# Kernel tuning notes

Measured on AMD Instinct MI355X. Metric: run time of the kernel, lower is better.

Reference implementation:

```python
import jax, jax.numpy as jnp
import numpy as np

NUM_HEAD = 16

def setup_inputs() -> dict:
    key = jax.random.key(0)
    ks = jax.random.split(key, 5)
    B, S, E = 2, 2048, 1024
    x = jax.random.normal(ks[0], (B, S, E), dtype=jnp.float32)
    w_qkv = jax.random.normal(ks[1], (3 * E, E), dtype=jnp.float32) * (E ** -0.5)
    b_qkv = jax.random.normal(ks[2], (3 * E,), dtype=jnp.float32) * 0.01
    w_out = jax.random.normal(ks[3], (E, E), dtype=jnp.float32) * (E ** -0.5)
    b_out = jax.random.normal(ks[4], (E,), dtype=jnp.float32) * 0.01
    return {"x": x, "w_qkv": w_qkv, "b_qkv": b_qkv, "w_out": w_out, "b_out": b_out}

def reference(x, w_qkv, b_qkv, w_out, b_out):
    B, S, E = x.shape
    H = NUM_HEAD
    D = E // H
    # fused QKV projection (torch Linear: x @ W^T + b)
    qkv = x @ w_qkv.T + b_qkv                       # [B, S, 3E]
    qkv = qkv.reshape(B, S, 3, H, D).transpose(2, 0, 3, 1, 4)  # [3, B, H, S, D]
    q, k, v = qkv[0], qkv[1], qkv[2]
    # NOTE: source scales by sqrt(embed_size), not sqrt(head_dim)
    scale = jnp.asarray(E, x.dtype) ** 0.5
    att = jnp.einsum('bhqd,bhkd->bhqk', q, k) / scale   # [B, H, S, S]
    # NOTE: source applies softmax over dim=1 (the head axis) — replicated faithfully
    att = jax.nn.softmax(att, axis=1)
    ctx = jnp.einsum('bhqk,bhkd->bhqd', att, v)         # [B, H, S, D]
    ctx = ctx.transpose(0, 2, 1, 3).reshape(B, S, E)    # [B, S, E]
    return ctx @ w_out.T + b_out
```

## Files before the change

kernel.cpp:

```cpp
#include <hip/hip_runtime.h>
#include <hip/hip_bf16.h>
#include <stdint.h>

typedef float  f32x4  __attribute__((ext_vector_type(4)));
typedef short  bf16x8 __attribute__((ext_vector_type(8)));
typedef short  bf16x4 __attribute__((ext_vector_type(4)));
typedef unsigned short u16x8 __attribute__((ext_vector_type(8)));

#define MFMA16(a, b, c) __builtin_amdgcn_mfma_f32_16x16x32_bf16((a), (b), (c), 0, 0, 0)

#if __has_builtin(__builtin_amdgcn_mfma_f32_16x16x16bf16_1k)
#define MFMA16K16(a, b, c) __builtin_amdgcn_mfma_f32_16x16x16bf16_1k((a), (b), (c), 0, 0, 0)
#else
__device__ __forceinline__ f32x4 mfma16k16_asm(bf16x4 a, bf16x4 b, f32x4 c) {
  f32x4 d;
  asm volatile("v_mfma_f32_16x16x16_bf16 %0, %1, %2, %3"
               : "=v"(d) : "v"(a), "v"(b), "v"(c));
  return d;
}
#define MFMA16K16(a, b, c) mfma16k16_asm((a), (b), (c))
#endif

__device__ __forceinline__ void gload16(const void* g, void* l) {
  __builtin_amdgcn_global_load_lds((const __attribute__((address_space(1))) void*)g,
                                   (__attribute__((address_space(3))) void*)l,
                                   16, 0, 0);
}

__device__ __forceinline__ unsigned short bf16bits(float f) {
  __hip_bfloat16 h = __float2bfloat16(f);
  return *(unsigned short*)&h;
}

__device__ __forceinline__ float bf2f(unsigned short u) {
  unsigned int x = ((unsigned int)u) << 16;
  return *(float*)&x;
}

__device__ __forceinline__ void block_sync_lds() {
  asm volatile("s_waitcnt lgkmcnt(0)" ::: "memory");
  __builtin_amdgcn_s_barrier();
  asm volatile("" ::: "memory");
}

__device__ __forceinline__ void fence_order() { asm volatile("" ::: "memory"); }

__global__ void cast_kernel(const float* __restrict__ s, __hip_bfloat16* __restrict__ d, int n4) {
  int i = blockIdx.x * blockDim.x + threadIdx.x;
  if (i < n4) {
    float4 v = ((const float4*)s)[i];
    ushort4 u;
    u.x = bf16bits(v.x); u.y = bf16bits(v.y); u.z = bf16bits(v.z); u.w = bf16bits(v.w);
    ((ushort4*)d)[i] = u;
  }
}

__global__ __launch_bounds__(256) void gemm_qkv_kernel(
    const __hip_bfloat16* __restrict__ A,
    const __hip_bfloat16* __restrict__ B,
    const float* __restrict__ bias,
    __hip_bfloat16* __restrict__ Qo,
    __hip_bfloat16* __restrict__ Ko,
    __hip_bfloat16* __restrict__ Vt) {
  const int K = 1024;
  __shared__ __align__(16) __hip_bfloat16 As[128 * 32];
  __shared__ __align__(16) __hip_bfloat16 Bs[128 * 32];
  const int t = threadIdx.x;
  const int lane = t & 63, wv = t >> 6;
  const int wm = (wv >> 1) * 64, wn = (wv & 1) * 64;
  const int lr = lane & 15, lq = lane >> 4;
  const int m0 = blockIdx.y * 128, n0 = blockIdx.x * 128;

  f32x4 acc[4][4] = {};

  const int arow = t >> 2;
  const int acol = (t & 3) * 8;
  const __hip_bfloat16* Ag = A + (long)(m0 + arow) * K + acol;
  const __hip_bfloat16* Bg = B + (long)(n0 + arow) * K + acol;
  __hip_bfloat16* Asl = As + t * 8;
  __hip_bfloat16* Bsl = Bs + t * 8;

  for (int kk = 0; kk < K; kk += 32) {
    gload16(Ag + kk, Asl);
    gload16(Ag + kk + 64 * K, Asl + 2048);
    gload16(Bg + kk, Bsl);
    gload16(Bg + kk + 64 * K, Bsl + 2048);
    __syncthreads();
    bf16x8 af[4], bf[4];
#pragma unroll
    for (int i = 0; i < 4; ++i)
      af[i] = *(const bf16x8*)&As[(wm + i * 16 + lr) * 32 + lq * 8];
#pragma unroll
    for (int j = 0; j < 4; ++j)
      bf[j] = *(const bf16x8*)&Bs[(wn + j * 16 + lr) * 32 + lq * 8];
#pragma unroll
    for (int i = 0; i < 4; ++i)
#pragma unroll
      for (int j = 0; j < 4; ++j)
        acc[i][j] = MFMA16(af[i], bf[j], acc[i][j]);
    __syncthreads();
  }

#pragma unroll
  for (int i = 0; i < 4; ++i) {
#pragma unroll
    for (int j = 0; j < 4; ++j) {
      int col = n0 + wn + j * 16 + lr;
      int tsel = col >> 10, rem = col & 1023;
      int h = rem >> 6, d = rem & 63;
      float bs = bias[col];
      int rowb = m0 + wm + i * 16 + lq * 4;
#pragma unroll
      for (int r = 0; r < 4; ++r) {
        int m = rowb + r;
        int b = m >> 11, sdx = m & 2047;
        __hip_bfloat16 v = __float2bfloat16(acc[i][j][r] + bs);
        long bh = (long)(b * 16 + h);
        if (tsel == 0)       Qo[(bh * 2048 + sdx) * 64 + d] = v;
        else if (tsel == 1)  Ko[(bh * 2048 + sdx) * 64 + d] = v;
        else                 Vt[((bh * 128 + (sdx >> 4)) * 64 + d) * 16 + (sdx & 15)] = v;
      }
    }
  }
}

__global__ __launch_bounds__(512, 2) void attn_kernel(
    const __hip_bfloat16* __restrict__ Q,
    const __hip_bfloat16* __restrict__ K,
    const __hip_bfloat16* __restrict__ Vt,
    __hip_bfloat16* __restrict__ part) {
  __shared__ __align__(16) __hip_bfloat16 KsA[16 * 16 * 64];
  __shared__ __align__(16) __hip_bfloat16 KsB[16 * 16 * 64];
  __shared__ __align__(16) float psum[2 * 8 * 16 * 16];

  const int t = threadIdx.x, lane = t & 63, wv = t >> 6;
  const int lr = lane & 15, lq = lane >> 4;
  const int h0 = wv * 2;
  const int combo = blockIdx.x & 7;
  const int b = combo & 1, chunk = combo >> 1;
  const int q0 = (blockIdx.x >> 3) * 32;
  const int k0 = chunk * 512;
  const float c = 0.03125f * 1.44269504f;
  const long bh16 = (long)(b * 16);
  const int rot = ((lq + lr) & 3) * 4;

  auto stageK = [&](__hip_bfloat16* dst, int kks) {
#pragma unroll
    for (int cc = 0; cc < 4; ++cc) {
      const int p = cc * 8192 + t * 16;
      const int rho = p >> 7;
      const int hh = rho >> 4, kl = rho & 15;
      const int g = ((p >> 4) & 7) ^ (rho & 7);
      const __hip_bfloat16* src = K + ((bh16 + hh) * 2048 + kks + kl) * 64 + g * 8;
      gload16(src, (char*)dst + p);
    }
    fence_order();
  };

  bf16x8 qf[2][2][2];
#pragma unroll
  for (int hh = 0; hh < 2; ++hh)
#pragma unroll
    for (int qt = 0; qt < 2; ++qt)
#pragma unroll
      for (int dh = 0; dh < 2; ++dh)
        qf[hh][qt][dh] = *(const bf16x8*)(
            Q + ((bh16 + h0 + hh) * 2048 + q0 + qt * 16 + lr) * 64 + dh * 32 + lq * 8);

  stageK(KsA, k0);
  asm volatile("s_waitcnt vmcnt(0)" ::: "memory");
  block_sync_lds();

  f32x4 ctx[2][2][4] = {};

  auto body = [&](const __hip_bfloat16* Kc, __hip_bfloat16* Kn, int kt) {
    const int kb = chunk * 32 + kt;
    bf16x4 vg[2][4];
#pragma unroll
    for (int hh = 0; hh < 2; ++hh) {
      const __hip_bfloat16* vb = Vt + ((bh16 + h0 + hh) * 128 + kb) * 1024;
#pragma unroll
      for (int dt = 0; dt < 4; ++dt)
        vg[hh][dt] = *(const bf16x4*)(vb + (dt * 16 + lr) * 16 + lq * 4);
    }
    if (kt < 31) stageK(Kn, k0 + kt * 16 + 16);
    f32x4 s[2][2];
    __builtin_amdgcn_s_setprio(1);
#pragma unroll
    for (int hh = 0; hh < 2; ++hh) {
      const int rho = (h0 + hh) * 16 + lr;
      const __hip_bfloat16* kr = Kc + rho * 64;
      bf16x8 kf0 = *(const bf16x8*)(kr + ((lq ^ (rho & 7)) << 3));
      bf16x8 kf1 = *(const bf16x8*)(kr + (((lq + 4) ^ (rho & 7)) << 3));
#pragma unroll
      for (int qt = 0; qt < 2; ++qt) {
        f32x4 a = {};
        a = MFMA16(kf0, qf[hh][qt][0], a);
        a = MFMA16(kf1, qf[hh][qt][1], a);
        s[hh][qt] = a;
      }
    }
    __builtin_amdgcn_s_setprio(0);
#pragma unroll
    for (int qt = 0; qt < 2; ++qt) {
      f32x4 pp;
#pragma unroll
      for (int r = 0; r < 4; ++r) {
        s[0][qt][r] = __builtin_amdgcn_exp2f(s[0][qt][r] * c);
        s[1][qt][r] = __builtin_amdgcn_exp2f(s[1][qt][r] * c);
        pp[r] = s[0][qt][r] + s[1][qt][r];
      }
      *(f32x4*)&psum[qt * 2048 + wv * 256 + lr * 16 + rot] = pp;
    }
    block_sync_lds();
    if (wv < 2) {
      f32x4 tot = {};
#pragma unroll
      for (int w2 = 0; w2 < 8; ++w2)
        tot += *(const f32x4*)&psum[wv * 2048 + w2 * 256 + lr * 16 + rot];
      f32x4 inv;
#pragma unroll
      for (int r = 0; r < 4; ++r) inv[r] = __builtin_amdgcn_rcpf(tot[r]);
      *(f32x4*)&psum[wv * 2048 + lr * 16 + rot] = inv;
    }
    asm volatile("s_waitcnt vmcnt(0)" ::: "memory");
    block_sync_lds();
    __builtin_amdgcn_s_setprio(1);
    f32x4 inv0 = *(const f32x4*)&psum[lr * 16 + rot];
    f32x4 inv1 = *(const f32x4*)&psum[2048 + lr * 16 + rot];
#pragma unroll
    for (int hh = 0; hh < 2; ++hh) {
#pragma unroll
      for (int qt = 0; qt < 2; ++qt) {
        const f32x4 iv = qt ? inv1 : inv0;
        bf16x4 p4;
#pragma unroll
        for (int r = 0; r < 4; ++r) p4[r] = (short)bf16bits(s[hh][qt][r] * iv[r]);
#pragma unroll
        for (int dt = 0; dt < 4; ++dt)
          ctx[hh][qt][dt] = MFMA16K16(vg[hh][dt], p4, ctx[hh][qt][dt]);
      }
    }
    __builtin_amdgcn_s_setprio(0);
  };

#pragma unroll 1
  for (int kp = 0; kp < 16; ++kp) {
    body(KsA, KsB, 2 * kp);
    body(KsB, KsA, 2 * kp + 1);
  }

  unsigned short* Pc = (unsigned short*)KsA;
#pragma unroll
  for (int qt = 0; qt < 2; ++qt) {
    if (qt) block_sync_lds();
#pragma unroll
    for (int hh = 0; hh < 2; ++hh) {
      const int h = h0 + hh;
#pragma unroll
      for (int dt = 0; dt < 4; ++dt) {
        bf16x4 pk;
#pragma unroll
        for (int r = 0; r < 4; ++r) pk[r] = (short)bf16bits(ctx[hh][qt][dt][r]);
        const int o = h * 128 + dt * 32 + lq * 8;
        *(bf16x4*)((char*)Pc + lr * 2048 + (o ^ ((lr & 7) << 4))) = pk;
      }
    }
    block_sync_lds();
    unsigned short* gbase = (unsigned short*)part +
        ((long)(chunk * 4096 + b * 2048 + q0 + qt * 16)) * 1024;
#pragma unroll
    for (int j = 0; j < 4; ++j) {
      int gf = (j * 512 + t) * 8;
      int q = gf >> 10, hd = gf & 1023;
      u16x8 v = *(const u16x8*)((char*)Pc + q * 2048 + ((hd * 2) ^ ((q & 7) << 4)));
      *(u16x8*)&gbase[gf] = v;
    }
  }
}

__global__ void reduce_cast_kernel(const unsigned short* __restrict__ part,
                                   __hip_bfloat16* __restrict__ dst) {
  int i = blockIdx.x * blockDim.x + threadIdx.x;
  const long S4 = (long)4096 * 1024 / 4;
  const ushort4* p = (const ushort4*)part;
  float sx = 0.f, sy = 0.f, sz = 0.f, sw = 0.f;
#pragma unroll
  for (int c = 0; c < 4; ++c) {
    ushort4 v = p[i + c * S4];
    sx += bf2f(v.x); sy += bf2f(v.y); sz += bf2f(v.z); sw += bf2f(v.w);
  }
  ushort4 u;
  u.x = bf16bits(sx); u.y = bf16bits(sy); u.z = bf16bits(sz); u.w = bf16bits(sw);
  ((ushort4*)dst)[i] = u;
}

__global__ __launch_bounds__(256) void gemm_out_kernel(
    const __hip_bfloat16* __restrict__ A,
    const __hip_bfloat16* __restrict__ B,
    const float* __restrict__ bias,
    float* __restrict__ out) {
  const int K = 1024;
  __shared__ __align__(16) __hip_bfloat16 As[128 * 32];
  __shared__ __align__(16) __hip_bfloat16 Bs[128 * 32];
  const int t = threadIdx.x;
  const int lane = t & 63, wv = t >> 6;
  const int wm = (wv >> 1) * 64, wn = (wv & 1) * 64;
  const int lr = lane & 15, lq = lane >> 4;
  const int m0 = blockIdx.y * 128, n0 = blockIdx.x * 128;

  f32x4 acc[4][4] = {};

  const int arow = t >> 2;
  const int acol = (t & 3) * 8;
  const __hip_bfloat16* Ag = A + (long)(m0 + arow) * K + acol;
  const __hip_bfloat16* Bg = B + (long)(n0 + arow) * K + acol;
  __hip_bfloat16* Asl = As + t * 8;
  __hip_bfloat16* Bsl = Bs + t * 8;

  for (int kk = 0; kk < K; kk += 32) {
    gload16(Ag + kk, Asl);
    gload16(Ag + kk + 64 * K, Asl + 2048);
    gload16(Bg + kk, Bsl);
    gload16(Bg + kk + 64 * K, Bsl + 2048);
    __syncthreads();
    bf16x8 af[4], bf[4];
#pragma unroll
    for (int i = 0; i < 4; ++i)
      af[i] = *(const bf16x8*)&As[(wm + i * 16 + lr) * 32 + lq * 8];
#pragma unroll
    for (int j = 0; j < 4; ++j)
      bf[j] = *(const bf16x8*)&Bs[(wn + j * 16 + lr) * 32 + lq * 8];
#pragma unroll
    for (int i = 0; i < 4; ++i)
#pragma unroll
      for (int j = 0; j < 4; ++j)
        acc[i][j] = MFMA16(af[i], bf[j], acc[i][j]);
    __syncthreads();
  }

#pragma unroll
  for (int i = 0; i < 4; ++i) {
#pragma unroll
    for (int j = 0; j < 4; ++j) {
      int col = n0 + wn + j * 16 + lr;
      float bs = bias[col];
      int rowb = m0 + wm + i * 16 + lq * 4;
#pragma unroll
      for (int r = 0; r < 4; ++r) {
        out[(long)(rowb + r) * 1024 + col] = acc[i][j][r] + bs;
      }
    }
  }
}

extern "C" void kernel_launch(void* const* d_in, const int* in_sizes, int n_in,
                              void* d_out, int out_size, void* d_ws, size_t ws_size,
                              hipStream_t stream) {
  const float* x     = (const float*)d_in[0];
  const float* w_qkv = (const float*)d_in[1];
  const float* b_qkv = (const float*)d_in[2];
  const float* w_out = (const float*)d_in[3];
  const float* b_out = (const float*)d_in[4];
  float* out = (float*)d_out;
  char* ws = (char*)d_ws;

  __hip_bfloat16* xb    = (__hip_bfloat16*)(ws);
  __hip_bfloat16* wqkvb = (__hip_bfloat16*)(ws + (8ul << 20));
  __hip_bfloat16* woutb = (__hip_bfloat16*)(ws + (14ul << 20));
  __hip_bfloat16* Qb    = (__hip_bfloat16*)(ws + (16ul << 20));
  __hip_bfloat16* Kb    = (__hip_bfloat16*)(ws + (24ul << 20));
  __hip_bfloat16* Vtb   = (__hip_bfloat16*)(ws + (32ul << 20));
  __hip_bfloat16* partb = (__hip_bfloat16*)(ws + (40ul << 20));
  __hip_bfloat16* ctxb  = (__hip_bfloat16*)(ws + (72ul << 20));

  cast_kernel<<<4096, 256, 0, stream>>>(x, xb, 4194304 / 4);
  cast_kernel<<<3072, 256, 0, stream>>>(w_qkv, wqkvb, 3145728 / 4);
  cast_kernel<<<1024, 256, 0, stream>>>(w_out, woutb, 1048576 / 4);
  gemm_qkv_kernel<<<dim3(24, 32), 256, 0, stream>>>(xb, wqkvb, b_qkv, Qb, Kb, Vtb);
  attn_kernel<<<512, 512, 0, stream>>>(Qb, Kb, Vtb, partb);
  reduce_cast_kernel<<<4096, 256, 0, stream>>>((const unsigned short*)partb, ctxb);
  gemm_out_kernel<<<dim3(8, 32), 256, 0, stream>>>(ctxb, woutb, b_out, out);
}
```

Before: 268.6 us.

## Load K fragments directly to registers with pre-tiled K layout, drop LDS staging

The QKV GEMM now writes K in a tiled layout that matches the MFMA fragment order, so the attention kernel loads K straight from global memory into registers instead of staging it through double-buffered LDS with global_load_lds. K and V fragments are register double-buffered and prefetched after the QK MFMAs. The softmax-over-heads reduction now has every wave compute the reciprocal sums itself, using double-buffered padded psum. That removes the second barrier and the vmcnt wait per step. This raises register pressure and issues more scattered global loads per wave in exchange for fewer barriers and less LDS traffic.

```diff
diff --git a/kernel.cpp b/kernel.cpp
--- a/kernel.cpp
+++ b/kernel.cpp
@@ -42,8 +42,6 @@
   __builtin_amdgcn_s_barrier();
   asm volatile("" ::: "memory");
 }
-
-__device__ __forceinline__ void fence_order() { asm volatile("" ::: "memory"); }
 
 __global__ void cast_kernel(const float* __restrict__ s, __hip_bfloat16* __restrict__ d, int n4) {
   int i = blockIdx.x * blockDim.x + threadIdx.x;
@@ -116,9 +114,14 @@
         int b = m >> 11, sdx = m & 2047;
         __hip_bfloat16 v = __float2bfloat16(acc[i][j][r] + bs);
         long bh = (long)(b * 16 + h);
-        if (tsel == 0)       Qo[(bh * 2048 + sdx) * 64 + d] = v;
-        else if (tsel == 1)  Ko[(bh * 2048 + sdx) * 64 + d] = v;
-        else                 Vt[((bh * 128 + (sdx >> 4)) * 64 + d) * 16 + (sdx & 15)] = v;
+        if (tsel == 0) {
+          Qo[(bh * 2048 + sdx) * 64 + d] = v;
+        } else if (tsel == 1) {
+          Ko[(bh * 128 + (sdx >> 4)) * 1024 + (d >> 5) * 512 +
+             ((d >> 3) & 3) * 128 + (sdx & 15) * 8 + (d & 7)] = v;
+        } else {
+          Vt[((bh * 128 + (sdx >> 4)) * 64 + d) * 16 + (sdx & 15)] = v;
+        }
       }
     }
   }
@@ -129,9 +132,8 @@
     const __hip_bfloat16* __restrict__ K,
     const __hip_bfloat16* __restrict__ Vt,
     __hip_bfloat16* __restrict__ part) {
-  __shared__ __align__(16) __hip_bfloat16 KsA[16 * 16 * 64];
-  __shared__ __align__(16) __hip_bfloat16 KsB[16 * 16 * 64];
-  __shared__ __align__(16) float psum[2 * 8 * 16 * 16];
+  __shared__ float psum[2][5120];
+  __shared__ __align__(16) unsigned short epi[16 * 1024];
 
   const int t = threadIdx.x, lane = t & 63, wv = t >> 6;
   const int lr = lane & 15, lq = lane >> 4;
@@ -139,23 +141,10 @@
   const int combo = blockIdx.x & 7;
   const int b = combo & 1, chunk = combo >> 1;
   const int q0 = (blockIdx.x >> 3) * 32;
-  const int k0 = chunk * 512;
+  const int kb0 = chunk * 32;
   const float c = 0.03125f * 1.44269504f;
   const long bh16 = (long)(b * 16);
-  const int rot = ((lq + lr) & 3) * 4;
-
-  auto stageK = [&](__hip_bfloat16* dst, int kks) {
-#pragma unroll
-    for (int cc = 0; cc < 4; ++cc) {
-      const int p = cc * 8192 + t * 16;
-      const int rho = p >> 7;
-      const int hh = rho >> 4, kl = rho & 15;
-      const int g = ((p >> 4) & 7) ^ (rho & 7);
-      const __hip_bfloat16* src = K + ((bh16 + hh) * 2048 + kks + kl) * 64 + g * 8;
-      gload16(src, (char*)dst + p);
-    }
-    fence_order();
-  };
+  const int poff = lr * 20 + lq * 4;
 
   bf16x8 qf[2][2][2];
 #pragma unroll
@@ -167,40 +156,43 @@
         qf[hh][qt][dh] = *(const bf16x8*)(
             Q + ((bh16 + h0 + hh) * 2048 + q0 + qt * 16 + lr) * 64 + dh * 32 + lq * 8);
 
-  stageK(KsA, k0);
-  asm volatile("s_waitcnt vmcnt(0)" ::: "memory");
-  block_sync_lds();
+  bf16x8 kfA[2][2], kfB[2][2];
+  bf16x4 vgA[2][4], vgB[2][4];
+
+  auto loadKV = [&](bf16x8 (&KF)[2][2], bf16x4 (&VG)[2][4], int kb) {
+#pragma unroll
+    for (int hh = 0; hh < 2; ++hh) {
+      const __hip_bfloat16* kptr =
+          K + ((bh16 + h0 + hh) * 128 + kb) * 1024 + lq * 128 + lr * 8;
+      KF[hh][0] = *(const bf16x8*)kptr;
+      KF[hh][1] = *(const bf16x8*)(kptr + 512);
+      const __hip_bfloat16* vptr =
+          Vt + ((bh16 + h0 + hh) * 128 + kb) * 1024 + lr * 16 + lq * 4;
+#pragma unroll
+      for (int dt = 0; dt < 4; ++dt)
+        VG[hh][dt] = *(const bf16x4*)(vptr + dt * 256);
+    }
+  };
+
+  loadKV(kfA, vgA, kb0);
 
   f32x4 ctx[2][2][4] = {};
 
-  auto body = [&](const __hip_bfloat16* Kc, __hip_bfloat16* Kn, int kt) {
-    const int kb = chunk * 32 + kt;
-    bf16x4 vg[2][4];
-#pragma unroll
-    for (int hh = 0; hh < 2; ++hh) {
-      const __hip_bfloat16* vb = Vt + ((bh16 + h0 + hh) * 128 + kb) * 1024;
-#pragma unroll
-      for (int dt = 0; dt < 4; ++dt)
-        vg[hh][dt] = *(const bf16x4*)(vb + (dt * 16 + lr) * 16 + lq * 4);
-    }
-    if (kt < 31) stageK(Kn, k0 + kt * 16 + 16);
+  auto body = [&](bf16x8 (&KF)[2][2], bf16x4 (&VG)[2][4],
+                  bf16x8 (&KFN)[2][2], bf16x4 (&VGN)[2][4], int kt, int par) {
     f32x4 s[2][2];
     __builtin_amdgcn_s_setprio(1);
 #pragma unroll
-    for (int hh = 0; hh < 2; ++hh) {
-      const int rho = (h0 + hh) * 16 + lr;
-      const __hip_bfloat16* kr = Kc + rho * 64;
-      bf16x8 kf0 = *(const bf16x8*)(kr + ((lq ^ (rho & 7)) << 3));
-      bf16x8 kf1 = *(const bf16x8*)(kr + (((lq + 4) ^ (rho & 7)) << 3));
+    for (int hh = 0; hh < 2; ++hh)
 #pragma unroll
       for (int qt = 0; qt < 2; ++qt) {
         f32x4 a = {};
-        a = MFMA16(kf0, qf[hh][qt][0], a);
-        a = MFMA16(kf1, qf[hh][qt][1], a);
+        a = MFMA16(KF[hh][0], qf[hh][qt][0], a);
+        a = MFMA16(KF[hh][1], qf[hh][qt][1], a);
         s[hh][qt] = a;
       }
-    }
     __builtin_amdgcn_s_setprio(0);
+    if (kt + 1 < 32) loadKV(KFN, VGN, kb0 + kt + 1);
 #pragma unroll
     for (int qt = 0; qt < 2; ++qt) {
       f32x4 pp;
@@ -210,47 +202,41 @@
         s[1][qt][r] = __builtin_amdgcn_exp2f(s[1][qt][r] * c);
         pp[r] = s[0][qt][r] + s[1][qt][r];
       }
-      *(f32x4*)&psum[qt * 2048 + wv * 256 + lr * 16 + rot] = pp;
+      *(f32x4*)&psum[par][qt * 2560 + wv * 320 + poff] = pp;
     }
     block_sync_lds();
-    if (wv < 2) {
+    f32x4 inv[2];
+#pragma unroll
+    for (int qt = 0; qt < 2; ++qt) {
       f32x4 tot = {};
 #pragma unroll
       for (int w2 = 0; w2 < 8; ++w2)
-        tot += *(const f32x4*)&psum[wv * 2048 + w2 * 256 + lr * 16 + rot];
-      f32x4 inv;
-#pragma unroll
-      for (int r = 0; r < 4; ++r) inv[r] = __builtin_amdgcn_rcpf(tot[r]);
-      *(f32x4*)&psum[wv * 2048 + lr * 16 + rot] = inv;
-    }
-    asm volatile("s_waitcnt vmcnt(0)" ::: "memory");
-    block_sync_lds();
+        tot += *(const f32x4*)&psum[par][qt * 2560 + w2 * 320 + poff];
+#pragma unroll
+      for (int r = 0; r < 4; ++r) inv[qt][r] = __builtin_amdgcn_rcpf(tot[r]);
+    }
     __builtin_amdgcn_s_setprio(1);
-    f32x4 inv0 = *(const f32x4*)&psum[lr * 16 + rot];
-    f32x4 inv1 = *(const f32x4*)&psum[2048 + lr * 16 + rot];
-#pragma unroll
-    for (int hh = 0; hh < 2; ++hh) {
+#pragma unroll
+    for (int hh = 0; hh < 2; ++hh)
 #pragma unroll
       for (int qt = 0; qt < 2; ++qt) {
-        const f32x4 iv = qt ? inv1 : inv0;
         bf16x4 p4;
 #pragma unroll
-        for (int r = 0; r < 4; ++r) p4[r] = (short)bf16bits(s[hh][qt][r] * iv[r]);
+        for (int r = 0; r < 4; ++r) p4[r] = (short)bf16bits(s[hh][qt][r] * inv[qt][r]);
 #pragma unroll
         for (int dt = 0; dt < 4; ++dt)
-          ctx[hh][qt][dt] = MFMA16K16(vg[hh][dt], p4, ctx[hh][qt][dt]);
-      }
-    }
+          ctx[hh][qt][dt] = MFMA16K16(VG[hh][dt], p4, ctx[hh][qt][dt]);
+      }
     __builtin_amdgcn_s_setprio(0);
   };
 
 #pragma unroll 1
   for (int kp = 0; kp < 16; ++kp) {
-    body(KsA, KsB, 2 * kp);
-    body(KsB, KsA, 2 * kp + 1);
-  }
-
-  unsigned short* Pc = (unsigned short*)KsA;
+    body(kfA, vgA, kfB, vgB, 2 * kp, 0);
+    body(kfB, vgB, kfA, vgA, 2 * kp + 1, 1);
+  }
+
+  unsigned short* Pc = epi;
 #pragma unroll
   for (int qt = 0; qt < 2; ++qt) {
     if (qt) block_sync_lds();
```

New measurement: 290.8 us. 1.08x slower.
